# Optimization experiments

Hardware: AMD Instinct MI355X
Metric: run time of the kernel (lower is better)

## Reference

```python
import jax, jax.numpy as jnp
import numpy as np

B = 2; DIM = 128; H = 48; W = 48
D2 = DIM // 2; DSTATE = 64; DCONV = 4


def _s6_params(key, d, n, k):
    ks = jax.random.split(key, 4)
    conv_w = jax.random.normal(ks[0], (d, k), dtype=jnp.float32) * 0.2
    conv_b = jnp.zeros((d,), jnp.float32)
    Wd = jax.random.normal(ks[1], (d, d), dtype=jnp.float32) / np.sqrt(d)
    bd = jnp.zeros((d,), jnp.float32)
    WB = jax.random.normal(ks[2], (d, n), dtype=jnp.float32) / np.sqrt(d)
    WC = jax.random.normal(ks[3], (d, n), dtype=jnp.float32) / np.sqrt(d)
    # S4D-real style init: A = -exp(Alog), Alog = log(1..n)
    Alog = jnp.log(jnp.broadcast_to(jnp.arange(1, n + 1, dtype=jnp.float32), (d, n)))
    Dp = jnp.ones((d,), jnp.float32)
    return conv_w, conv_b, Wd, bd, WB, WC, Alog, Dp


def setup_inputs() -> dict:
    key = jax.random.key(0)
    ks = jax.random.split(key, 5)
    x = jax.random.normal(ks[0], (B, DIM, H, W), dtype=jnp.float32)
    Wx = jax.random.normal(ks[1], (DIM, DIM), dtype=jnp.float32) / np.sqrt(DIM)
    bx = jnp.zeros((DIM,), jnp.float32)
    Wp = jax.random.normal(ks[2], (DIM, DIM), dtype=jnp.float32) / np.sqrt(DIM)
    bp = jnp.zeros((DIM,), jnp.float32)
    f = _s6_params(ks[3], D2, DSTATE, DCONV)
    r = _s6_params(ks[4], D2, DSTATE, DCONV)
    d = {"x": x, "Wx": Wx, "bx": bx, "Wp": Wp, "bp": bp}
    fn = ["f_conv_w", "f_conv_b", "f_Wd", "f_bd", "f_WB", "f_WC", "f_Alog", "f_D"]
    rn = ["r_conv_w", "r_conv_b", "r_Wd", "r_bd", "r_WB", "r_WC", "r_Alog", "r_D"]
    d.update(dict(zip(fn, f)))
    d.update(dict(zip(rn, r)))
    return d


def _s6(u, conv_w, conv_b, Wd, bd, WB, WC, Alog, Dp):
    # u: (b, d, L) selective state-space scan (S6)
    b, d, L = u.shape
    K = conv_w.shape[1]
    up = jnp.pad(u, ((0, 0), (0, 0), (K - 1, 0)))  # causal depthwise conv, kernel K
    xc = sum(conv_w[:, k][None, :, None] * up[:, :, k:k + L] for k in range(K))
    xc = jax.nn.silu(xc + conv_b[None, :, None])
    xt = xc.transpose(0, 2, 1)  # (b, L, d)
    delta = jax.nn.softplus(xt @ Wd + bd)          # (b, L, d)
    Bm = xt @ WB                                   # (b, L, n)
    Cm = xt @ WC                                   # (b, L, n)
    A = -jnp.exp(Alog)                             # (d, n)
    dA = jnp.exp(delta[..., None] * A)             # (b, L, d, n)
    dBx = (delta * xt)[..., None] * Bm[:, :, None, :]  # (b, L, d, n)

    def combine(c1, c2):
        a1, b1 = c1
        a2, b2 = c2
        return a2 * a1, a2 * b1 + b2

    _, h = jax.lax.associative_scan(combine, (dA, dBx), axis=1)  # (b, L, d, n)
    y = jnp.einsum('bldn,bln->bld', h, Cm) + Dp * xt
    return y.transpose(0, 2, 1)  # (b, d, L)


def reference(x, Wx, bx, Wp, bp,
              f_conv_w, f_conv_b, f_Wd, f_bd, f_WB, f_WC, f_Alog, f_D,
              r_conv_w, r_conv_b, r_Wd, r_bd, r_WB, r_WC, r_Alog, r_D):
    n, c, h, w = x.shape
    t = jnp.einsum('oc,bchw->bohw', Wx, x) + bx[None, :, None, None]
    seq = t.reshape(n, c, h * w)
    half = c // 2
    xF = seq[:, :half]
    xR = jnp.flip(seq[:, half:], axis=-1)
    yF = _s6(xF, f_conv_w, f_conv_b, f_Wd, f_bd, f_WB, f_WC, f_Alog, f_D)
    yR = jnp.flip(_s6(xR, r_conv_w, r_conv_b, r_Wd, r_bd, r_WB, r_WC, r_Alog, r_D), axis=-1)
    y = jnp.concatenate([yF, yR], axis=1).reshape(n, c, h, w)
    return jnp.einsum('oc,bchw->bohw', Wp, y) + bp[None, :, None, None]
```

## Files before the change

### kernel.cpp

```cpp
#include <hip/hip_runtime.h>

#define BN     2
#define DIMC   128
#define D2C    64
#define LCONST 2304
#define NS     4
#define TCH    16
#define NCH    144
#define NT     38
#define TW     61

__global__ __launch_bounds__(256) void ka_inconv(const float* __restrict__ x,
                                                 const float* __restrict__ Wx,
                                                 const float* __restrict__ bx,
                                                 const float* __restrict__ fcw,
                                                 const float* __restrict__ fcb,
                                                 const float* __restrict__ rcw,
                                                 const float* __restrict__ rcb,
                                                 float* __restrict__ xc) {
    int wid = __builtin_amdgcn_readfirstlane((blockIdx.x * 256 + threadIdx.x) >> 6);
    int j   = threadIdx.x & 63;
    int tile = wid % NT;
    int sg   = wid / NT;
    int dg   = sg & 15, s = sg >> 4;
    int b    = s & 1, rev = s >> 1;
    int d0   = dg * 4;
    int o0   = d0 + (rev ? 64 : 0);
    int lg   = tile * TW + j - 3;
    int lc   = min(max(lg, 0), LCONST - 1);
    int p    = rev ? (LCONST - 1 - lc) : lc;
    const float* xb = x + (size_t)(b * DIMC) * LCONST + p;
    float um[4];
    #pragma unroll
    for (int i = 0; i < 4; ++i) um[i] = bx[o0 + i];
    #pragma unroll 8
    for (int c = 0; c < DIMC; ++c) {
        float xv = xb[(size_t)c * LCONST];
        #pragma unroll
        for (int i = 0; i < 4; ++i)
            um[i] = fmaf(Wx[(o0 + i) * DIMC + c], xv, um[i]);
    }
    if (lg < 0) {
        #pragma unroll
        for (int i = 0; i < 4; ++i) um[i] = 0.f;
    }
    const float* cw  = rev ? rcw : fcw;
    const float* cbp = rev ? rcb : fcb;
    float res[4];
    #pragma unroll
    for (int i = 0; i < 4; ++i) {
        float u1 = __shfl_up(um[i], 1);
        float u2 = __shfl_up(um[i], 2);
        float u3 = __shfl_up(um[i], 3);
        const float* w = cw + (d0 + i) * 4;
        float z = cbp[d0 + i];
        z = fmaf(w[3], um[i], z);
        z = fmaf(w[2], u1, z);
        z = fmaf(w[1], u2, z);
        z = fmaf(w[0], u3, z);
        res[i] = z / (1.f + __expf(-z));
    }
    if (j >= 3 && lg < LCONST) {
        *(float4*)(xc + ((size_t)s * LCONST + lg) * 64 + d0) =
            make_float4(res[0], res[1], res[2], res[3]);
    }
}

__global__ __launch_bounds__(512) void k4_projscan(const float* __restrict__ xc,
                                                   const float* __restrict__ fWd, const float* __restrict__ fbd,
                                                   const float* __restrict__ fWB,
                                                   const float* __restrict__ rWd, const float* __restrict__ rbd,
                                                   const float* __restrict__ rWB,
                                                   float* __restrict__ Sd,
                                                   float* __restrict__ E) {
    __shared__ float xs[TCH * 64], dls[TCH * 64], Bs[TCH * 64];
    int c = blockIdx.x % NCH;
    int s = blockIdx.x / NCH;
    int tid  = threadIdx.x;
    int lane = tid & 63;
    int w    = tid >> 6;
    int n0   = w * 8;
    size_t base = ((size_t)s * LCONST + c * TCH) * 64;
    xs[tid]       = xc[base + tid];
    xs[tid + 512] = xc[base + tid + 512];
    __syncthreads();
    int dirR = s >> 1;
    const float* Wd = dirR ? rWd : fWd;
    const float* WB = dirR ? rWB : fWB;
    float bdv = (dirR ? rbd : fbd)[lane];
    #pragma unroll
    for (int rr = 0; rr < 2; ++rr) {
        int r = (w << 1) + rr;
        const float* xr = xs + r * 64;
        float ad = 0.f, ab = 0.f;
        #pragma unroll 8
        for (int d = 0; d < 64; ++d) {
            float xv = xr[d];
            ad = fmaf(xv, Wd[d * 64 + lane], ad);
            ab = fmaf(xv, WB[d * 64 + lane], ab);
        }
        float a = ad + bdv;
        dls[r * 64 + lane] = (a > 20.f) ? a : log1pf(__expf(a));
        Bs[r * 64 + lane]  = ab;
    }
    __syncthreads();
    float h[8];
    #pragma unroll
    for (int i = 0; i < 8; ++i) h[i] = 0.f;
    float sdsum = 0.f;
    #pragma unroll 4
    for (int t = 0; t < TCH; ++t) {
        float dv = dls[t * 64 + lane];
        float xv = xs[t * 64 + lane];
        sdsum += dv;
        float q  = __expf(-dv);
        float du = dv * xv;
        float4 b0 = *(const float4*)(Bs + t * 64 + n0);
        float4 b1 = *(const float4*)(Bs + t * 64 + n0 + 4);
        float q2 = q * q, q4 = q2 * q2;
        float pw0 = __expf(-(float)(n0 + 1) * dv);
        float pw1 = pw0 * q, pw2 = pw0 * q2, pw3 = pw1 * q2;
        h[0] = fmaf(pw0, h[0], du * b0.x);
        h[1] = fmaf(pw1, h[1], du * b0.y);
        h[2] = fmaf(pw2, h[2], du * b0.z);
        h[3] = fmaf(pw3, h[3], du * b0.w);
        pw0 *= q4; pw1 *= q4; pw2 *= q4; pw3 *= q4;
        h[4] = fmaf(pw0, h[4], du * b1.x);
        h[5] = fmaf(pw1, h[5], du * b1.y);
        h[6] = fmaf(pw2, h[6], du * b1.z);
        h[7] = fmaf(pw3, h[7], du * b1.w);
    }
    int eb = (s * NCH + c) * 64;
    #pragma unroll
    for (int i = 0; i < 8; ++i)
        E[(size_t)(eb + n0 + i) * 64 + lane] = h[i];
    if (w == 0) Sd[eb + lane] = sdsum;
}

__global__ __launch_bounds__(128) void k5_chunkscan(const float* __restrict__ Sd,
                                                    const float* __restrict__ E,
                                                    float* __restrict__ H0) {
    int q = blockIdx.x * 128 + threadIdx.x;
    int s = q >> 12;
    int n = (q >> 6) & 63;
    int d = q & 63;
    float hr = 0.f;
    float cn = -(float)(n + 1);
    for (int cb = 0; cb < NCH; cb += 8) {
        float sdv[8], ev[8];
        #pragma unroll
        for (int i = 0; i < 8; ++i) {
            int c = cb + i;
            sdv[i] = Sd[(s * NCH + c) * 64 + d];
            ev[i]  = E[((size_t)(s * NCH + c) * 64 + n) * 64 + d];
        }
        #pragma unroll
        for (int i = 0; i < 8; ++i) {
            H0[((size_t)(s * NCH + cb + i) * 64 + n) * 64 + d] = hr;
            hr = fmaf(__expf(cn * sdv[i]), hr, ev[i]);
        }
    }
}

__global__ __launch_bounds__(512) void k6_projscan(const float* __restrict__ xc,
                                                   const float* __restrict__ fWd, const float* __restrict__ fbd,
                                                   const float* __restrict__ fWB, const float* __restrict__ fWC,
                                                   const float* __restrict__ rWd, const float* __restrict__ rbd,
                                                   const float* __restrict__ rWB, const float* __restrict__ rWC,
                                                   const float* __restrict__ H0,
                                                   const float* __restrict__ fD,
                                                   const float* __restrict__ rD,
                                                   float* __restrict__ yT) {
    __shared__ float xs[TCH * 64], dls[TCH * 64], Bs[TCH * 64], Cs[TCH * 64];
    __shared__ float yred[8 * TCH * 64];
    int c = blockIdx.x % NCH;
    int s = blockIdx.x / NCH;
    int tid  = threadIdx.x;
    int lane = tid & 63;
    int w    = tid >> 6;
    int n0   = w * 8;
    size_t base = ((size_t)s * LCONST + c * TCH) * 64;
    xs[tid]       = xc[base + tid];
    xs[tid + 512] = xc[base + tid + 512];
    __syncthreads();
    int dirR = s >> 1;
    const float* Wd = dirR ? rWd : fWd;
    const float* WB = dirR ? rWB : fWB;
    const float* WC = dirR ? rWC : fWC;
    float bdv = (dirR ? rbd : fbd)[lane];
    #pragma unroll
    for (int rr = 0; rr < 2; ++rr) {
        int r = (w << 1) + rr;
        const float* xr = xs + r * 64;
        float ad = 0.f, ab = 0.f, ac = 0.f;
        #pragma unroll 8
        for (int d = 0; d < 64; ++d) {
            float xv = xr[d];
            ad = fmaf(xv, Wd[d * 64 + lane], ad);
            ab = fmaf(xv, WB[d * 64 + lane], ab);
            ac = fmaf(xv, WC[d * 64 + lane], ac);
        }
        float a = ad + bdv;
        dls[r * 64 + lane] = (a > 20.f) ? a : log1pf(__expf(a));
        Bs[r * 64 + lane]  = ab;
        Cs[r * 64 + lane]  = ac;
    }
    int eb = (s * NCH + c) * 64;
    float h[8];
    #pragma unroll
    for (int i = 0; i < 8; ++i)
        h[i] = H0[(size_t)(eb + n0 + i) * 64 + lane];
    __syncthreads();
    float* yw = yred + w * (TCH * 64) + lane;
    #pragma unroll 4
    for (int t = 0; t < TCH; ++t) {
        float dv = dls[t * 64 + lane];
        float xv = xs[t * 64 + lane];
        float q  = __expf(-dv);
        float du = dv * xv;
        float4 b0 = *(const float4*)(Bs + t * 64 + n0);
        float4 b1 = *(const float4*)(Bs + t * 64 + n0 + 4);
        float4 c0 = *(const float4*)(Cs + t * 64 + n0);
        float4 c1 = *(const float4*)(Cs + t * 64 + n0 + 4);
        float q2 = q * q, q4 = q2 * q2;
        float pw0 = __expf(-(float)(n0 + 1) * dv);
        float pw1 = pw0 * q, pw2 = pw0 * q2, pw3 = pw1 * q2;
        float y0, y1, y2, y3;
        h[0] = fmaf(pw0, h[0], du * b0.x);  y0 = h[0] * c0.x;
        h[1] = fmaf(pw1, h[1], du * b0.y);  y1 = h[1] * c0.y;
        h[2] = fmaf(pw2, h[2], du * b0.z);  y2 = h[2] * c0.z;
        h[3] = fmaf(pw3, h[3], du * b0.w);  y3 = h[3] * c0.w;
        pw0 *= q4; pw1 *= q4; pw2 *= q4; pw3 *= q4;
        h[4] = fmaf(pw0, h[4], du * b1.x);  y0 = fmaf(h[4], c1.x, y0);
        h[5] = fmaf(pw1, h[5], du * b1.y);  y1 = fmaf(h[5], c1.y, y1);
        h[6] = fmaf(pw2, h[6], du * b1.z);  y2 = fmaf(h[6], c1.z, y2);
        h[7] = fmaf(pw3, h[7], du * b1.w);  y3 = fmaf(h[7], c1.w, y3);
        yw[t * 64] = (y0 + y1) + (y2 + y3);
    }
    __syncthreads();
    int b = s & 1;
    float Dv = (dirR ? rD : fD)[lane];
    #pragma unroll
    for (int e = 0; e < 2; ++e) {
        int idx = tid + e * 512;
        int t = idx >> 6;
        float yv = ((yred[0 * TCH * 64 + idx] + yred[1 * TCH * 64 + idx])
                  + (yred[2 * TCH * 64 + idx] + yred[3 * TCH * 64 + idx]))
                 + ((yred[4 * TCH * 64 + idx] + yred[5 * TCH * 64 + idx])
                  + (yred[6 * TCH * 64 + idx] + yred[7 * TCH * 64 + idx]));
        float xv = xs[idx];
        yv = fmaf(Dv, xv, yv);
        int l    = c * TCH + t;
        int lout = dirR ? (LCONST - 1 - l) : l;
        int ch   = dirR ? (64 + lane) : lane;
        yT[((size_t)b * DIMC + ch) * LCONST + lout] = yv;
    }
}

__global__ __launch_bounds__(256) void k7_outproj(const float* __restrict__ yT,
                                                  const float* __restrict__ Wp,
                                                  const float* __restrict__ bp,
                                                  float* __restrict__ out) {
    int idx = blockIdx.x * 256 + threadIdx.x;
    int p   = idx % LCONST;
    int r   = __builtin_amdgcn_readfirstlane(idx / LCONST);
    int og  = r & 31;
    int b   = r >> 5;
    int o0  = og * 4;
    float acc[4];
    #pragma unroll
    for (int i = 0; i < 4; ++i) acc[i] = bp[o0 + i];
    const float* yb = yT + (size_t)(b * DIMC) * LCONST + p;
    #pragma unroll 8
    for (int c = 0; c < DIMC; ++c) {
        float yv = yb[(size_t)c * LCONST];
        #pragma unroll
        for (int i = 0; i < 4; ++i)
            acc[i] = fmaf(Wp[(o0 + i) * DIMC + c], yv, acc[i]);
    }
    #pragma unroll
    for (int i = 0; i < 4; ++i)
        out[((size_t)b * DIMC + o0 + i) * LCONST + p] = acc[i];
}

extern "C" void kernel_launch(void* const* d_in, const int* in_sizes, int n_in,
                              void* d_out, int out_size, void* d_ws, size_t ws_size,
                              hipStream_t stream) {
    const float* x   = (const float*)d_in[0];
    const float* Wx  = (const float*)d_in[1];
    const float* bx  = (const float*)d_in[2];
    const float* Wp  = (const float*)d_in[3];
    const float* bp  = (const float*)d_in[4];
    const float* fcw = (const float*)d_in[5];
    const float* fcb = (const float*)d_in[6];
    const float* fWd = (const float*)d_in[7];
    const float* fbd = (const float*)d_in[8];
    const float* fWB = (const float*)d_in[9];
    const float* fWC = (const float*)d_in[10];
    const float* fD  = (const float*)d_in[12];
    const float* rcw = (const float*)d_in[13];
    const float* rcb = (const float*)d_in[14];
    const float* rWd = (const float*)d_in[15];
    const float* rbd = (const float*)d_in[16];
    const float* rWB = (const float*)d_in[17];
    const float* rWC = (const float*)d_in[18];
    const float* rD  = (const float*)d_in[20];

    float* ws = (float*)d_ws;
    const size_t SEG = (size_t)NS * D2C * LCONST;
    float* xcb = ws;
    float* yT  = ws + SEG;
    float* Sd  = ws + 2 * SEG;
    float* E   = Sd + (size_t)NS * NCH * 64;
    float* H0  = E + (size_t)NS * NCH * 4096;
    float* out = (float*)d_out;

    ka_inconv<<<(NS * 16 * NT * 64) / 256, 256, 0, stream>>>(x, Wx, bx, fcw, fcb, rcw, rcb, xcb);
    k4_projscan<<<NS * NCH, 512, 0, stream>>>(xcb, fWd, fbd, fWB, rWd, rbd, rWB, Sd, E);
    k5_chunkscan<<<128, 128, 0, stream>>>(Sd, E, H0);
    k6_projscan<<<NS * NCH, 512, 0, stream>>>(xcb, fWd, fbd, fWB, fWC, rWd, rbd, rWB, rWC,
                                              H0, fD, rD, yT);
    k7_outproj<<<(BN * 32 * LCONST) / 256, 256, 0, stream>>>(yT, Wp, bp, out);
}
```

Measured before the change: 172.2 us.

## Fuse output projection into scan kernel with atomic accumulation

Removes the separate out-projection kernel and the yT intermediate. Each scan block now multiplies its 16-timestep by 64-channel y tile by the matching half of Wp and atomically adds the partial results into the output. The forward and reverse directions both add into the same output. The output is zeroed inside the chunk-scan kernel beforehand (9 float4 per thread covers the full output). This saves a launch and a global round trip, but adds atomics, shuffle reductions and redundant Wp loads per block, and makes float summation order nondeterministic.

```diff
diff --git a/kernel.cpp b/kernel.cpp
--- a/kernel.cpp
+++ b/kernel.cpp
@@ -139,8 +139,15 @@
 
 __global__ __launch_bounds__(128) void k5_chunkscan(const float* __restrict__ Sd,
                                                     const float* __restrict__ E,
-                                                    float* __restrict__ H0) {
+                                                    float* __restrict__ H0,
+                                                    float* __restrict__ out) {
     int q = blockIdx.x * 128 + threadIdx.x;
+    {
+        float4 z = make_float4(0.f, 0.f, 0.f, 0.f);
+        float4* o4 = (float4*)out;
+        #pragma unroll
+        for (int i = 0; i < 9; ++i) o4[q + i * 16384] = z;
+    }
     int s = q >> 12;
     int n = (q >> 6) & 63;
     int d = q & 63;
@@ -170,9 +177,12 @@
                                                    const float* __restrict__ H0,
                                                    const float* __restrict__ fD,
                                                    const float* __restrict__ rD,
-                                                   float* __restrict__ yT) {
+                                                   const float* __restrict__ Wp,
+                                                   const float* __restrict__ bp,
+                                                   float* __restrict__ out) {
     __shared__ float xs[TCH * 64], dls[TCH * 64], Bs[TCH * 64], Cs[TCH * 64];
     __shared__ float yred[8 * TCH * 64];
+    float* ys = yred;
     int c = blockIdx.x % NCH;
     int s = blockIdx.x / NCH;
     int tid  = threadIdx.x;
@@ -238,49 +248,66 @@
         yw[t * 64] = (y0 + y1) + (y2 + y3);
     }
     __syncthreads();
-    int b = s & 1;
     float Dv = (dirR ? rD : fD)[lane];
-    #pragma unroll
-    for (int e = 0; e < 2; ++e) {
-        int idx = tid + e * 512;
-        int t = idx >> 6;
-        float yv = ((yred[0 * TCH * 64 + idx] + yred[1 * TCH * 64 + idx])
-                  + (yred[2 * TCH * 64 + idx] + yred[3 * TCH * 64 + idx]))
-                 + ((yred[4 * TCH * 64 + idx] + yred[5 * TCH * 64 + idx])
-                  + (yred[6 * TCH * 64 + idx] + yred[7 * TCH * 64 + idx]));
-        float xv = xs[idx];
-        yv = fmaf(Dv, xv, yv);
-        int l    = c * TCH + t;
-        int lout = dirR ? (LCONST - 1 - l) : l;
-        int ch   = dirR ? (64 + lane) : lane;
-        yT[((size_t)b * DIMC + ch) * LCONST + lout] = yv;
-    }
-}
-
-__global__ __launch_bounds__(256) void k7_outproj(const float* __restrict__ yT,
-                                                  const float* __restrict__ Wp,
-                                                  const float* __restrict__ bp,
-                                                  float* __restrict__ out) {
-    int idx = blockIdx.x * 256 + threadIdx.x;
-    int p   = idx % LCONST;
-    int r   = __builtin_amdgcn_readfirstlane(idx / LCONST);
-    int og  = r & 31;
-    int b   = r >> 5;
-    int o0  = og * 4;
-    float acc[4];
-    #pragma unroll
-    for (int i = 0; i < 4; ++i) acc[i] = bp[o0 + i];
-    const float* yb = yT + (size_t)(b * DIMC) * LCONST + p;
-    #pragma unroll 8
-    for (int c = 0; c < DIMC; ++c) {
-        float yv = yb[(size_t)c * LCONST];
-        #pragma unroll
-        for (int i = 0; i < 4; ++i)
-            acc[i] = fmaf(Wp[(o0 + i) * DIMC + c], yv, acc[i]);
-    }
-    #pragma unroll
-    for (int i = 0; i < 4; ++i)
-        out[((size_t)b * DIMC + o0 + i) * LCONST + p] = acc[i];
+    float yv0, yv1;
+    {
+        int idx = tid;
+        yv0 = ((yred[0 * TCH * 64 + idx] + yred[1 * TCH * 64 + idx])
+             + (yred[2 * TCH * 64 + idx] + yred[3 * TCH * 64 + idx]))
+            + ((yred[4 * TCH * 64 + idx] + yred[5 * TCH * 64 + idx])
+             + (yred[6 * TCH * 64 + idx] + yred[7 * TCH * 64 + idx]));
+        yv0 = fmaf(Dv, xs[idx], yv0);
+    }
+    {
+        int idx = tid + 512;
+        yv1 = ((yred[0 * TCH * 64 + idx] + yred[1 * TCH * 64 + idx])
+             + (yred[2 * TCH * 64 + idx] + yred[3 * TCH * 64 + idx]))
+            + ((yred[4 * TCH * 64 + idx] + yred[5 * TCH * 64 + idx])
+             + (yred[6 * TCH * 64 + idx] + yred[7 * TCH * 64 + idx]));
+        yv1 = fmaf(Dv, xs[idx], yv1);
+    }
+    __syncthreads();
+    {
+        int t0 = tid >> 6;
+        ys[t0 * 68 + lane]       = yv0;
+        ys[(t0 + 8) * 68 + lane] = yv1;
+    }
+    __syncthreads();
+    int b  = s & 1;
+    int px = lane & 15;
+    int cg = lane >> 4;
+    int t_sel = dirR ? (15 - px) : px;
+    int p_out = (dirR ? (NCH - 1 - c) : c) * TCH + px;
+    const float* ysrow = ys + t_sel * 68 + cg * 16;
+    float4 ya = *(const float4*)(ysrow);
+    float4 yb = *(const float4*)(ysrow + 4);
+    float4 yc = *(const float4*)(ysrow + 8);
+    float4 yd = *(const float4*)(ysrow + 12);
+    const float* WpB = Wp + (dirR ? 64 : 0) + cg * 16;
+    float* outB = out + (size_t)b * DIMC * LCONST + p_out;
+    #pragma unroll 4
+    for (int r = 0; r < 16; ++r) {
+        int och = r * 8 + w;
+        const float* wr = WpB + och * DIMC;
+        float4 wa = *(const float4*)(wr);
+        float4 wb = *(const float4*)(wr + 4);
+        float4 wc = *(const float4*)(wr + 8);
+        float4 wd = *(const float4*)(wr + 12);
+        float acc = wa.x * ya.x;
+        acc = fmaf(wa.y, ya.y, acc); acc = fmaf(wa.z, ya.z, acc); acc = fmaf(wa.w, ya.w, acc);
+        acc = fmaf(wb.x, yb.x, acc); acc = fmaf(wb.y, yb.y, acc);
+        acc = fmaf(wb.z, yb.z, acc); acc = fmaf(wb.w, yb.w, acc);
+        acc = fmaf(wc.x, yc.x, acc); acc = fmaf(wc.y, yc.y, acc);
+        acc = fmaf(wc.z, yc.z, acc); acc = fmaf(wc.w, yc.w, acc);
+        acc = fmaf(wd.x, yd.x, acc); acc = fmaf(wd.y, yd.y, acc);
+        acc = fmaf(wd.z, yd.z, acc); acc = fmaf(wd.w, yd.w, acc);
+        acc += __shfl_xor(acc, 16);
+        acc += __shfl_xor(acc, 32);
+        if (cg == 0) {
+            float v = dirR ? acc : (acc + bp[och]);
+            atomicAdd(outB + (size_t)och * LCONST, v);
+        }
+    }
 }
 
 extern "C" void kernel_launch(void* const* d_in, const int* in_sizes, int n_in,
@@ -309,7 +336,6 @@
     float* ws = (float*)d_ws;
     const size_t SEG = (size_t)NS * D2C * LCONST;
     float* xcb = ws;
-    float* yT  = ws + SEG;
     float* Sd  = ws + 2 * SEG;
     float* E   = Sd + (size_t)NS * NCH * 64;
     float* H0  = E + (size_t)NS * NCH * 4096;
@@ -317,8 +343,7 @@
 
     ka_inconv<<<(NS * 16 * NT * 64) / 256, 256, 0, stream>>>(x, Wx, bx, fcw, fcb, rcw, rcb, xcb);
     k4_projscan<<<NS * NCH, 512, 0, stream>>>(xcb, fWd, fbd, fWB, rWd, rbd, rWB, Sd, E);
-    k5_chunkscan<<<128, 128, 0, stream>>>(Sd, E, H0);
+    k5_chunkscan<<<128, 128, 0, stream>>>(Sd, E, H0, out);
     k6_projscan<<<NS * NCH, 512, 0, stream>>>(xcb, fWd, fbd, fWB, fWC, rWd, rbd, rWB, rWC,
-                                              H0, fD, rD, yT);
-    k7_outproj<<<(BN * 32 * LCONST) / 256, 256, 0, stream>>>(yT, Wp, bp, out);
-}
+                                              H0, fD, rD, Wp, bp, out);
+}
```

Measured after the change: 177.6 us. 3.2% more time.

## Compute delta/B/C projections once in k4 and reuse them from global in k6

Applied to the files above, without the earlier changes.

The first projection-scan kernel now computes delta, B and C for each chunk. It spreads the three matrices over six waves, each handling 8 rows with register-blocked accumulators, and writes the results to global workspace. The second kernel drops its duplicate projection GEMV and shared staging, reading delta, B, C and x straight from global memory in the scan loop. This removes redundant projection arithmetic and a barrier. In exchange it adds extra global writes and reads, and two waves in k4 sit idle during the projection.

```diff
diff --git a/kernel.cpp b/kernel.cpp
--- a/kernel.cpp
+++ b/kernel.cpp
@@ -68,11 +68,14 @@
 
 __global__ __launch_bounds__(512) void k4_projscan(const float* __restrict__ xc,
                                                    const float* __restrict__ fWd, const float* __restrict__ fbd,
-                                                   const float* __restrict__ fWB,
+                                                   const float* __restrict__ fWB, const float* __restrict__ fWC,
                                                    const float* __restrict__ rWd, const float* __restrict__ rbd,
-                                                   const float* __restrict__ rWB,
+                                                   const float* __restrict__ rWB, const float* __restrict__ rWC,
                                                    float* __restrict__ Sd,
-                                                   float* __restrict__ E) {
+                                                   float* __restrict__ E,
+                                                   float* __restrict__ dlG,
+                                                   float* __restrict__ BG,
+                                                   float* __restrict__ CG) {
     __shared__ float xs[TCH * 64], dls[TCH * 64], Bs[TCH * 64];
     int c = blockIdx.x % NCH;
     int s = blockIdx.x / NCH;
@@ -85,23 +88,47 @@
     xs[tid + 512] = xc[base + tid + 512];
     __syncthreads();
     int dirR = s >> 1;
-    const float* Wd = dirR ? rWd : fWd;
-    const float* WB = dirR ? rWB : fWB;
-    float bdv = (dirR ? rbd : fbd)[lane];
-    #pragma unroll
-    for (int rr = 0; rr < 2; ++rr) {
-        int r = (w << 1) + rr;
-        const float* xr = xs + r * 64;
-        float ad = 0.f, ab = 0.f;
+    if (w < 6) {
+        int m  = w >> 1;
+        int rh = w & 1;
+        const float* W = (m == 0) ? (dirR ? rWd : fWd)
+                       : (m == 1) ? (dirR ? rWB : fWB)
+                                  : (dirR ? rWC : fWC);
+        float acc[8];
+        #pragma unroll
+        for (int i = 0; i < 8; ++i) acc[i] = 0.f;
+        const float* xrow = xs + rh * 8 * 64;
         #pragma unroll 8
         for (int d = 0; d < 64; ++d) {
-            float xv = xr[d];
-            ad = fmaf(xv, Wd[d * 64 + lane], ad);
-            ab = fmaf(xv, WB[d * 64 + lane], ab);
+            float wv = W[d * 64 + lane];
+            #pragma unroll
+            for (int r = 0; r < 8; ++r)
+                acc[r] = fmaf(xrow[r * 64 + d], wv, acc[r]);
         }
-        float a = ad + bdv;
-        dls[r * 64 + lane] = (a > 20.f) ? a : log1pf(__expf(a));
-        Bs[r * 64 + lane]  = ab;
+        if (m == 0) {
+            float bdv = (dirR ? rbd : fbd)[lane];
+            #pragma unroll
+            for (int r = 0; r < 8; ++r) {
+                int rr = rh * 8 + r;
+                float a = acc[r] + bdv;
+                float v = (a > 20.f) ? a : log1pf(__expf(a));
+                dls[rr * 64 + lane]      = v;
+                dlG[base + rr * 64 + lane] = v;
+            }
+        } else if (m == 1) {
+            #pragma unroll
+            for (int r = 0; r < 8; ++r) {
+                int rr = rh * 8 + r;
+                Bs[rr * 64 + lane]      = acc[r];
+                BG[base + rr * 64 + lane] = acc[r];
+            }
+        } else {
+            #pragma unroll
+            for (int r = 0; r < 8; ++r) {
+                int rr = rh * 8 + r;
+                CG[base + rr * 64 + lane] = acc[r];
+            }
+        }
     }
     __syncthreads();
     float h[8];
@@ -162,16 +189,14 @@
     }
 }
 
-__global__ __launch_bounds__(512) void k6_projscan(const float* __restrict__ xc,
-                                                   const float* __restrict__ fWd, const float* __restrict__ fbd,
-                                                   const float* __restrict__ fWB, const float* __restrict__ fWC,
-                                                   const float* __restrict__ rWd, const float* __restrict__ rbd,
-                                                   const float* __restrict__ rWB, const float* __restrict__ rWC,
-                                                   const float* __restrict__ H0,
-                                                   const float* __restrict__ fD,
-                                                   const float* __restrict__ rD,
-                                                   float* __restrict__ yT) {
-    __shared__ float xs[TCH * 64], dls[TCH * 64], Bs[TCH * 64], Cs[TCH * 64];
+__global__ __launch_bounds__(512) void k6_scan(const float* __restrict__ xc,
+                                               const float* __restrict__ dlG,
+                                               const float* __restrict__ BG,
+                                               const float* __restrict__ CG,
+                                               const float* __restrict__ H0,
+                                               const float* __restrict__ fD,
+                                               const float* __restrict__ rD,
+                                               float* __restrict__ yT) {
     __shared__ float yred[8 * TCH * 64];
     int c = blockIdx.x % NCH;
     int s = blockIdx.x / NCH;
@@ -179,49 +204,24 @@
     int lane = tid & 63;
     int w    = tid >> 6;
     int n0   = w * 8;
+    int dirR = s >> 1;
     size_t base = ((size_t)s * LCONST + c * TCH) * 64;
-    xs[tid]       = xc[base + tid];
-    xs[tid + 512] = xc[base + tid + 512];
-    __syncthreads();
-    int dirR = s >> 1;
-    const float* Wd = dirR ? rWd : fWd;
-    const float* WB = dirR ? rWB : fWB;
-    const float* WC = dirR ? rWC : fWC;
-    float bdv = (dirR ? rbd : fbd)[lane];
-    #pragma unroll
-    for (int rr = 0; rr < 2; ++rr) {
-        int r = (w << 1) + rr;
-        const float* xr = xs + r * 64;
-        float ad = 0.f, ab = 0.f, ac = 0.f;
-        #pragma unroll 8
-        for (int d = 0; d < 64; ++d) {
-            float xv = xr[d];
-            ad = fmaf(xv, Wd[d * 64 + lane], ad);
-            ab = fmaf(xv, WB[d * 64 + lane], ab);
-            ac = fmaf(xv, WC[d * 64 + lane], ac);
-        }
-        float a = ad + bdv;
-        dls[r * 64 + lane] = (a > 20.f) ? a : log1pf(__expf(a));
-        Bs[r * 64 + lane]  = ab;
-        Cs[r * 64 + lane]  = ac;
-    }
     int eb = (s * NCH + c) * 64;
     float h[8];
     #pragma unroll
     for (int i = 0; i < 8; ++i)
         h[i] = H0[(size_t)(eb + n0 + i) * 64 + lane];
-    __syncthreads();
     float* yw = yred + w * (TCH * 64) + lane;
     #pragma unroll 4
     for (int t = 0; t < TCH; ++t) {
-        float dv = dls[t * 64 + lane];
-        float xv = xs[t * 64 + lane];
+        float dv = dlG[base + t * 64 + lane];
+        float xv = xc[base + t * 64 + lane];
         float q  = __expf(-dv);
         float du = dv * xv;
-        float4 b0 = *(const float4*)(Bs + t * 64 + n0);
-        float4 b1 = *(const float4*)(Bs + t * 64 + n0 + 4);
-        float4 c0 = *(const float4*)(Cs + t * 64 + n0);
-        float4 c1 = *(const float4*)(Cs + t * 64 + n0 + 4);
+        float4 b0 = *(const float4*)(BG + base + t * 64 + n0);
+        float4 b1 = *(const float4*)(BG + base + t * 64 + n0 + 4);
+        float4 c0 = *(const float4*)(CG + base + t * 64 + n0);
+        float4 c1 = *(const float4*)(CG + base + t * 64 + n0 + 4);
         float q2 = q * q, q4 = q2 * q2;
         float pw0 = __expf(-(float)(n0 + 1) * dv);
         float pw1 = pw0 * q, pw2 = pw0 * q2, pw3 = pw1 * q2;
@@ -248,7 +248,7 @@
                   + (yred[2 * TCH * 64 + idx] + yred[3 * TCH * 64 + idx]))
                  + ((yred[4 * TCH * 64 + idx] + yred[5 * TCH * 64 + idx])
                   + (yred[6 * TCH * 64 + idx] + yred[7 * TCH * 64 + idx]));
-        float xv = xs[idx];
+        float xv = xc[base + idx];
         yv = fmaf(Dv, xv, yv);
         int l    = c * TCH + t;
         int lout = dirR ? (LCONST - 1 - l) : l;
@@ -313,12 +313,15 @@
     float* Sd  = ws + 2 * SEG;
     float* E   = Sd + (size_t)NS * NCH * 64;
     float* H0  = E + (size_t)NS * NCH * 4096;
+    float* dlG = H0 + (size_t)NS * NCH * 4096;
+    float* BG  = dlG + SEG;
+    float* CG  = BG + SEG;
     float* out = (float*)d_out;
 
     ka_inconv<<<(NS * 16 * NT * 64) / 256, 256, 0, stream>>>(x, Wx, bx, fcw, fcb, rcw, rcb, xcb);
-    k4_projscan<<<NS * NCH, 512, 0, stream>>>(xcb, fWd, fbd, fWB, rWd, rbd, rWB, Sd, E);
+    k4_projscan<<<NS * NCH, 512, 0, stream>>>(xcb, fWd, fbd, fWB, fWC, rWd, rbd, rWB, rWC,
+                                              Sd, E, dlG, BG, CG);
     k5_chunkscan<<<128, 128, 0, stream>>>(Sd, E, H0);
-    k6_projscan<<<NS * NCH, 512, 0, stream>>>(xcb, fWd, fbd, fWB, fWC, rWd, rbd, rWB, rWC,
-                                              H0, fD, rD, yT);
+    k6_scan<<<NS * NCH, 512, 0, stream>>>(xcb, dlG, BG, CG, H0, fD, rD, yT);
     k7_outproj<<<(BN * 32 * LCONST) / 256, 256, 0, stream>>>(yT, Wp, bp, out);
 }
```

Measured after the change: 162.6 us. -5.6%, faster.
